# Kernel optimization log

Measured on AMD Instinct MI355X. Metric: run time of the kernel, lower is better.

Reference implementation:

```python
import jax, jax.numpy as jnp
import numpy as np

B, TK, NK, H = 64, 512, 256, 512

def _masked_renorm_softmax(scores, mask):
    # softmax over last dim, multiply by mask, renormalize (as in the torch code)
    p = jax.nn.softmax(scores, axis=-1) * mask
    return p / jnp.sum(p, axis=-1, keepdims=True)

def setup_inputs() -> dict:
    key = jax.random.key(0)
    ks = jax.random.split(key, 14)
    s = 0.02
    return {
        "s_t_hat": jax.random.normal(ks[0], (B, 2 * H), jnp.float32),
        "encoder_outputs_token": jax.random.normal(ks[1], (B, TK, H), jnp.float32),
        "encoder_outputs_node": jax.random.normal(ks[2], (B, NK, H), jnp.float32),
        "node_to_token": jax.random.randint(ks[3], (B, TK), 0, NK),
        "enc_padding_mask_token": jnp.ones((B, TK), jnp.float32),
        "enc_padding_mask_node": jnp.ones((B, NK), jnp.float32),
        "graph": jax.random.uniform(ks[4], (B, NK, NK), jnp.float32),
        "flow": jax.random.uniform(ks[5], (B, NK), jnp.float32),
        # parameters (Linear weights stored as [in, out]; x @ W == torch Linear)
        "W_c": jax.random.normal(ks[6], (H,), jnp.float32) * s,          # Linear(1, H)
        "W_tok": jax.random.normal(ks[7], (H, H), jnp.float32) * s,      # encode_proj_token
        "W_node": jax.random.normal(ks[8], (H, H), jnp.float32) * s,     # encode_proj_node
        "W_dec": jax.random.normal(ks[9], (2 * H, H), jnp.float32) * s,  # decode_proj
        "b_dec": jnp.zeros((H,), jnp.float32),
        "v_tok": jax.random.normal(ks[10], (H,), jnp.float32) * s,       # v_token
        "v_node": jax.random.normal(ks[11], (H,), jnp.float32) * s,      # v_node
    }

def reference(s_t_hat, encoder_outputs_token, encoder_outputs_node, node_to_token,
              enc_padding_mask_token, enc_padding_mask_node, graph, flow,
              W_c, W_tok, W_node, W_dec, b_dec, v_tok, v_node):
    # projections
    enc_tok_feat = jnp.einsum('bth,hk->btk', encoder_outputs_token, W_tok)   # [B,TK,H]
    enc_node_feat = jnp.einsum('bnh,hk->bnk', encoder_outputs_node, W_node)  # [B,NK,H]
    dec_fea = s_t_hat @ W_dec + b_dec                                        # [B,H]
    flow_feat = flow[..., None] * W_c                                        # [B,NK,H]

    # node attention
    e_node = jnp.tanh(enc_node_feat + dec_fea[:, None, :] + flow_feat)
    scores_node = jnp.einsum('bnh,h->bn', e_node, v_node)                    # [B,NK]
    attn_dist_node = _masked_renorm_softmax(scores_node, enc_padding_mask_node)

    # gather node attention onto tokens via node_to_token indices
    gathered = jnp.take_along_axis(attn_dist_node, node_to_token, axis=1)    # [B,TK]
    attn_dist_node_to_token = _masked_renorm_softmax(gathered, enc_padding_mask_token)

    # token attention
    e_tok = jnp.tanh(enc_tok_feat + dec_fea[:, None, :])
    scores_tok = jnp.einsum('bth,h->bt', e_tok, v_tok)                       # [B,TK]
    attn_dist_token = _masked_renorm_softmax(scores_tok, enc_padding_mask_token)

    # mix and context
    final_attn = 0.5 * attn_dist_token + 0.5 * attn_dist_node_to_token      # [B,TK]
    c_t = jnp.einsum('bt,bth->bh', final_attn, encoder_outputs_token)        # [B,H]

    # multi-hop graph diffusion of node attention
    zero_hop = attn_dist_node                                                # [B,NK]
    one_hop = jnp.einsum('bn,bnm->bm', zero_hop, graph)
    two_hop = jnp.einsum('bn,bnm->bm', one_hop, graph)
    flow_out = (zero_hop + one_hop + two_hop) * 0.33333

    return (c_t, final_attn, attn_dist_node, flow_out)
```

## Files before the change

### kernel.cpp

```cpp
#include <hip/hip_runtime.h>
#include <math.h>

constexpr int kB = 64;
constexpr int kTK = 512;
constexpr int kNK = 256;
constexpr int kH = 512;

typedef float f32x4 __attribute__((ext_vector_type(4)));
typedef __bf16 bf16x8 __attribute__((ext_vector_type(8)));
typedef unsigned short u16x8 __attribute__((ext_vector_type(8)));

__device__ __forceinline__ unsigned short f32_to_bf16(float f) {
  unsigned int u = __float_as_uint(f);
  u += 0x7fffu + ((u >> 16) & 1u);
  return (unsigned short)(u >> 16);
}

__device__ __forceinline__ float tanh_fast(float x) {
  float e = __builtin_amdgcn_exp2f(x * 2.8853900817779268f);
  return 1.0f - 2.0f * __builtin_amdgcn_rcpf(e + 1.0f);
}

__global__ __launch_bounds__(256) void transpose_w_kernel(
    const float* __restrict__ Wtok, const float* __restrict__ Wnode,
    unsigned short* __restrict__ WtokT, unsigned short* __restrict__ WnodeT) {
  const float* W = blockIdx.z ? Wnode : Wtok;
  unsigned short* T = blockIdx.z ? WnodeT : WtokT;
  __shared__ float tile[32][33];
  const int tx = threadIdx.x, ty = threadIdx.y;
  const int bx = blockIdx.x, by = blockIdx.y;
#pragma unroll
  for (int i = 0; i < 4; ++i)
    tile[ty + 8 * i][tx] = W[(size_t)(by * 32 + ty + 8 * i) * kH + bx * 32 + tx];
  __syncthreads();
#pragma unroll
  for (int i = 0; i < 4; ++i)
    T[(size_t)(bx * 32 + ty + 8 * i) * kH + by * 32 + tx] =
        f32_to_bf16(tile[tx][ty + 8 * i]);
}

__global__ __launch_bounds__(512) void dec_partial_kernel(
    const float* __restrict__ s_t_hat, const float* __restrict__ W_dec,
    float* __restrict__ part) {
  const int b = blockIdx.x, s = blockIdx.y, h = threadIdx.x;
  __shared__ float sh[128];
  if (h < 128) sh[h] = s_t_hat[(size_t)b * (2 * kH) + s * 128 + h];
  __syncthreads();
  float acc = 0.f;
  const float* w = W_dec + (size_t)(s * 128) * kH + h;
#pragma unroll 8
  for (int k = 0; k < 128; ++k) acc = fmaf(sh[k], w[(size_t)k * kH], acc);
  part[(size_t)(b * 8 + s) * kH + h] = acc;
}

__global__ __launch_bounds__(512) void dec_reduce_kernel(
    const float* __restrict__ part, const float* __restrict__ b_dec,
    float* __restrict__ dec_fea) {
  const int b = blockIdx.x, h = threadIdx.x;
  float acc = b_dec[h];
#pragma unroll
  for (int s = 0; s < 8; ++s) acc += part[(size_t)(b * 8 + s) * kH + h];
  dec_fea[b * kH + h] = acc;
}

template <int ROWS, bool IS_NODE>
__global__ __launch_bounds__(512, 2) void scores_kernel(
    const float* __restrict__ A,
    const unsigned short* __restrict__ WT,
    const float* __restrict__ dec_fea,
    const float* __restrict__ flow,
    const float* __restrict__ W_c,
    const float* __restrict__ v,
    float* __restrict__ scores)
{
  constexpr int TILES_PER_B = ROWS / 64;
  const int b = blockIdx.x / TILES_PER_B;
  const int row0 = (blockIdx.x % TILES_PER_B) * 64;
  const int tid = threadIdx.x;
  const int wave = tid >> 6;
  const int lane = tid & 63;
  const int quad = lane >> 4;
  const int l15 = lane & 15;
  const int n0 = wave * 64;

  __shared__ __align__(16) unsigned short As[2][4096];
  __shared__ float red[8][64];

  const f32x4 fzero = {0.f, 0.f, 0.f, 0.f};
  f32x4 acc[4][4];
#pragma unroll
  for (int i = 0; i < 4; ++i)
#pragma unroll
    for (int j = 0; j < 4; ++j) acc[i][j] = fzero;

  const int sr = tid >> 3;
  const int kq = tid & 7;
  const int slot = (((kq >> 2) * 4 + (sr >> 4)) * 64 + (kq & 3) * 16 + (sr & 15)) * 8;
  const float* aptr = A + ((size_t)(b * ROWS + row0 + sr)) * kH + kq * 8;

  auto stage = [&](int kc, int buf) {
    float4 a0 = *(const float4*)(aptr + kc * 64);
    float4 a1 = *(const float4*)(aptr + kc * 64 + 4);
    u16x8 h;
    h[0] = f32_to_bf16(a0.x); h[1] = f32_to_bf16(a0.y);
    h[2] = f32_to_bf16(a0.z); h[3] = f32_to_bf16(a0.w);
    h[4] = f32_to_bf16(a1.x); h[5] = f32_to_bf16(a1.y);
    h[6] = f32_to_bf16(a1.z); h[7] = f32_to_bf16(a1.w);
    *(u16x8*)&As[buf][slot] = h;
  };

  const unsigned short* bbase = WT + (size_t)(n0 + l15) * kH + quad * 8;
  auto load_b = [&](bf16x8 (&dst)[2][4], int kc) {
#pragma unroll
    for (int kh = 0; kh < 2; ++kh)
#pragma unroll
      for (int ni = 0; ni < 4; ++ni)
        dst[kh][ni] =
            *(const bf16x8*)(bbase + (size_t)(ni * 16) * kH + kc * 64 + kh * 32);
  };

  bf16x8 bcur[2][4];
  stage(0, 0);
  load_b(bcur, 0);
  __syncthreads();

#pragma unroll
  for (int kc = 0; kc < 8; ++kc) {
    bf16x8 bnxt[2][4];
    if (kc < 7) {
      load_b(bnxt, kc + 1);
      stage(kc + 1, (kc + 1) & 1);
    }
    bf16x8 afr[2][4];
#pragma unroll
    for (int kh = 0; kh < 2; ++kh)
#pragma unroll
      for (int mi = 0; mi < 4; ++mi)
        afr[kh][mi] = *(const bf16x8*)&As[kc & 1][((kh * 4 + mi) * 64 + lane) * 8];
#pragma unroll
    for (int kh = 0; kh < 2; ++kh)
#pragma unroll
      for (int mi = 0; mi < 4; ++mi)
#pragma unroll
        for (int ni = 0; ni < 4; ++ni)
          acc[mi][ni] = __builtin_amdgcn_mfma_f32_16x16x32_bf16(
              afr[kh][mi], bcur[kh][ni], acc[mi][ni], 0, 0, 0);
    if (kc < 7) {
#pragma unroll
      for (int kh = 0; kh < 2; ++kh)
#pragma unroll
        for (int ni = 0; ni < 4; ++ni) bcur[kh][ni] = bnxt[kh][ni];
      __syncthreads();
    }
  }

  float dec4[4], vv4[4], wc4[4];
#pragma unroll
  for (int ni = 0; ni < 4; ++ni) {
    const int col = n0 + 16 * ni + l15;
    dec4[ni] = dec_fea[b * kH + col];
    vv4[ni] = v[col];
    if constexpr (IS_NODE) wc4[ni] = W_c[col]; else wc4[ni] = 0.f;
  }
#pragma unroll
  for (int mi = 0; mi < 4; ++mi) {
#pragma unroll
    for (int reg = 0; reg < 4; ++reg) {
      const int row = 16 * mi + quad * 4 + reg;
      float fl = 0.f;
      if constexpr (IS_NODE) fl = flow[b * kNK + row0 + row];
      float p = 0.f;
#pragma unroll
      for (int ni = 0; ni < 4; ++ni) {
        float val = acc[mi][ni][reg] + dec4[ni];
        if constexpr (IS_NODE) val = fmaf(fl, wc4[ni], val);
        p += tanh_fast(val) * vv4[ni];
      }
#pragma unroll
      for (int off = 1; off < 16; off <<= 1) p += __shfl_xor(p, off, 64);
      if (l15 == 0) red[wave][row] = p;
    }
  }
  __syncthreads();
  if (tid < 64) {
    float s = 0.f;
#pragma unroll
    for (int w = 0; w < 8; ++w) s += red[w][tid];
    scores[b * ROWS + row0 + tid] = s;
  }
}

__device__ __forceinline__ float block_sum_512(float v, float* rbuf) {
#pragma unroll
  for (int off = 32; off >= 1; off >>= 1) v += __shfl_xor(v, off, 64);
  if ((threadIdx.x & 63) == 0) rbuf[threadIdx.x >> 6] = v;
  __syncthreads();
  float s = rbuf[0];
#pragma unroll
  for (int w = 1; w < 8; ++w) s += rbuf[w];
  __syncthreads();
  return s;
}

__global__ __launch_bounds__(512) void softmax_mix_kernel(
    const float* __restrict__ scores_node, const float* __restrict__ scores_tok,
    const int* __restrict__ node_to_token,
    const float* __restrict__ mask_tok, const float* __restrict__ mask_node,
    float* __restrict__ out_final, float* __restrict__ out_attn_node) {
  const int b = blockIdx.x, tid = threadIdx.x;
  __shared__ float an_sh[kNK];
  __shared__ float rbuf[8];

  float en = 0.f;
  if (tid < kNK)
    en = expf(scores_node[b * kNK + tid]) * mask_node[b * kNK + tid];
  float sn = block_sum_512(en, rbuf);
  float an = en / sn;
  if (tid < kNK) {
    an_sh[tid] = an;
    out_attn_node[b * kNK + tid] = an;
  }
  __syncthreads();

  const float mt = mask_tok[b * kTK + tid];
  const int idx = node_to_token[b * kTK + tid];
  float eg = expf(an_sh[idx]) * mt;
  float sg = block_sum_512(eg, rbuf);
  float an2t = eg / sg;

  float et = expf(scores_tok[b * kTK + tid]) * mt;
  float st = block_sum_512(et, rbuf);
  float at = et / st;

  out_final[b * kTK + tid] = 0.5f * (at + an2t);
}

__global__ __launch_bounds__(512) void ct_partial_kernel(
    const float* __restrict__ final_attn, const float* __restrict__ enc_tok,
    float* __restrict__ ctp) {
  const int s = blockIdx.x, b = blockIdx.y, h = threadIdx.x;
  __shared__ float fa[64];
  if (h < 64) fa[h] = final_attn[b * kTK + s * 64 + h];
  __syncthreads();
  float acc = 0.f;
  const float* base = enc_tok + ((size_t)(b * kTK + s * 64)) * kH + h;
#pragma unroll 8
  for (int t = 0; t < 64; ++t) acc = fmaf(fa[t], base[(size_t)t * kH], acc);
  ctp[(size_t)(b * 8 + s) * kH + h] = acc;
}

__global__ __launch_bounds__(512) void ct_reduce_kernel(
    const float* __restrict__ ctp, float* __restrict__ out_ct) {
  const int b = blockIdx.x, h = threadIdx.x;
  float acc = 0.f;
#pragma unroll
  for (int s = 0; s < 8; ++s) acc += ctp[(size_t)(b * 8 + s) * kH + h];
  out_ct[b * kH + h] = acc;
}

__global__ __launch_bounds__(256) void flow1_kernel(
    const float* __restrict__ attn_node, const float* __restrict__ graph,
    float* __restrict__ fp1) {
  const int s = blockIdx.x, b = blockIdx.y, m = threadIdx.x;
  __shared__ float z[32];
  if (m < 32) z[m] = attn_node[b * kNK + s * 32 + m];
  __syncthreads();
  float acc = 0.f;
  const float* g = graph + ((size_t)(b * kNK + s * 32)) * kNK + m;
#pragma unroll 8
  for (int n = 0; n < 32; ++n) acc = fmaf(z[n], g[(size_t)n * kNK], acc);
  fp1[(b * 8 + s) * kNK + m] = acc;
}

__global__ __launch_bounds__(256) void flow3_kernel(
    const float* __restrict__ fp1, const float* __restrict__ graph,
    float* __restrict__ fp2) {
  const int s = blockIdx.x, b = blockIdx.y, m = threadIdx.x;
  __shared__ float one[32];
  if (m < 32) {
    float o = 0.f;
#pragma unroll
    for (int sp = 0; sp < 8; ++sp) o += fp1[(b * 8 + sp) * kNK + s * 32 + m];
    one[m] = o;
  }
  __syncthreads();
  float acc = 0.f;
  const float* g = graph + ((size_t)(b * kNK + s * 32)) * kNK + m;
#pragma unroll 8
  for (int n = 0; n < 32; ++n) acc = fmaf(one[n], g[(size_t)n * kNK], acc);
  fp2[(b * 8 + s) * kNK + m] = acc;
}

__global__ __launch_bounds__(256) void flow4_kernel(
    const float* __restrict__ fp1, const float* __restrict__ fp2,
    const float* __restrict__ attn_node, float* __restrict__ out_flow) {
  const int b = blockIdx.x, m = threadIdx.x;
  float one = 0.f, two = 0.f;
#pragma unroll
  for (int s = 0; s < 8; ++s) {
    one += fp1[(b * 8 + s) * kNK + m];
    two += fp2[(b * 8 + s) * kNK + m];
  }
  out_flow[b * kNK + m] = (attn_node[b * kNK + m] + one + two) * 0.33333f;
}

extern "C" void kernel_launch(void* const* d_in, const int* in_sizes, int n_in,
                              void* d_out, int out_size, void* d_ws, size_t ws_size,
                              hipStream_t stream) {
  (void)in_sizes; (void)n_in; (void)out_size; (void)ws_size;
  const float* s_t_hat  = (const float*)d_in[0];
  const float* enc_tok  = (const float*)d_in[1];
  const float* enc_node = (const float*)d_in[2];
  const int*   n2t      = (const int*)d_in[3];
  const float* mask_tok = (const float*)d_in[4];
  const float* mask_nd  = (const float*)d_in[5];
  const float* graph    = (const float*)d_in[6];
  const float* flow     = (const float*)d_in[7];
  const float* W_c      = (const float*)d_in[8];
  const float* W_tok    = (const float*)d_in[9];
  const float* W_node   = (const float*)d_in[10];
  const float* W_dec    = (const float*)d_in[11];
  const float* b_dec    = (const float*)d_in[12];
  const float* v_tok    = (const float*)d_in[13];
  const float* v_node   = (const float*)d_in[14];

  float* out = (float*)d_out;
  float* out_ct        = out;
  float* out_final     = out + kB * kH;
  float* out_attn_node = out + 2 * kB * kH;
  float* out_flow      = out_attn_node + kB * kNK;

  float* ws = (float*)d_ws;
  float* dec_fea_buf = ws;
  float* scores_tok  = ws + 32768;
  float* scores_node = ws + 65536;
  float* fp1         = ws + 81920;
  float* fp2         = ws + 212992;
  float* dec_part    = ws + 344064;
  float* ctp         = dec_part;
  unsigned short* WtokT  = (unsigned short*)(ws + 606208);
  unsigned short* WnodeT = WtokT + kH * kH;

  transpose_w_kernel<<<dim3(16, 16, 2), dim3(32, 8), 0, stream>>>(
      W_tok, W_node, WtokT, WnodeT);
  dec_partial_kernel<<<dim3(kB, 8), 512, 0, stream>>>(s_t_hat, W_dec, dec_part);
  dec_reduce_kernel<<<kB, 512, 0, stream>>>(dec_part, b_dec, dec_fea_buf);
  scores_kernel<kTK, false><<<kB * kTK / 64, 512, 0, stream>>>(
      enc_tok, WtokT, dec_fea_buf, nullptr, nullptr, v_tok, scores_tok);
  scores_kernel<kNK, true><<<kB * kNK / 64, 512, 0, stream>>>(
      enc_node, WnodeT, dec_fea_buf, flow, W_c, v_node, scores_node);
  softmax_mix_kernel<<<kB, 512, 0, stream>>>(scores_node, scores_tok, n2t,
                                             mask_tok, mask_nd, out_final, out_attn_node);
  ct_partial_kernel<<<dim3(8, kB), 512, 0, stream>>>(out_final, enc_tok, ctp);
  ct_reduce_kernel<<<kB, 512, 0, stream>>>(ctp, out_ct);
  flow1_kernel<<<dim3(8, kB), 256, 0, stream>>>(out_attn_node, graph, fp1);
  flow3_kernel<<<dim3(8, kB), 256, 0, stream>>>(fp1, graph, fp2);
  flow4_kernel<<<kB, 256, 0, stream>>>(fp1, fp2, out_attn_node, out_flow);
}
```

Measured before the change: 248.1 us.

## Fuse launches: merge prep, scores, context and graph-diffusion kernels with atomics

Cuts the launch count from eleven to five. The weight transpose is merged with the decoder partial GEMV. Token and node score GEMMs run in one 1024-thread kernel with a narrower per-wave N tile and a finer K pipeline, and the dec reduction is folded into its epilogue. The context reduction and two-hop graph diffusion are fused into two kernels that accumulate flow_out with atomicAdd, and bf16 rounding is simplified to round-half-up. The aim is to remove launch gaps and small reduction kernels. In exchange, atomics make the flow sum order nondeterministic and the rounding change slightly alters numerics.

```diff
diff --git a/kernel.cpp b/kernel.cpp
--- a/kernel.cpp
+++ b/kernel.cpp
@@ -5,15 +5,15 @@
 constexpr int kTK = 512;
 constexpr int kNK = 256;
 constexpr int kH = 512;
+constexpr int kTokBlocks = kB * kTK / 64;
+constexpr int kNodeBlocks = kB * kNK / 64;
 
 typedef float f32x4 __attribute__((ext_vector_type(4)));
 typedef __bf16 bf16x8 __attribute__((ext_vector_type(8)));
 typedef unsigned short u16x8 __attribute__((ext_vector_type(8)));
 
 __device__ __forceinline__ unsigned short f32_to_bf16(float f) {
-  unsigned int u = __float_as_uint(f);
-  u += 0x7fffu + ((u >> 16) & 1u);
-  return (unsigned short)(u >> 16);
+  return (unsigned short)((__float_as_uint(f) + 0x8000u) >> 16);
 }
 
 __device__ __forceinline__ float tanh_fast(float x) {
@@ -21,161 +21,155 @@
   return 1.0f - 2.0f * __builtin_amdgcn_rcpf(e + 1.0f);
 }
 
-__global__ __launch_bounds__(256) void transpose_w_kernel(
+__device__ __forceinline__ void lds_barrier() {
+  __builtin_amdgcn_s_waitcnt(0xC07F);
+  __builtin_amdgcn_s_barrier();
+}
+
+__global__ __launch_bounds__(256) void prep_kernel(
     const float* __restrict__ Wtok, const float* __restrict__ Wnode,
-    unsigned short* __restrict__ WtokT, unsigned short* __restrict__ WnodeT) {
-  const float* W = blockIdx.z ? Wnode : Wtok;
-  unsigned short* T = blockIdx.z ? WnodeT : WtokT;
-  __shared__ float tile[32][33];
-  const int tx = threadIdx.x, ty = threadIdx.y;
-  const int bx = blockIdx.x, by = blockIdx.y;
+    unsigned short* __restrict__ WtokT, unsigned short* __restrict__ WnodeT,
+    const float* __restrict__ s_t_hat, const float* __restrict__ W_dec,
+    float* __restrict__ dec_part) {
+  __shared__ float sm[32 * 33];
+  const int tid = threadIdx.x;
+  if (blockIdx.x < 512) {
+    const int idx = blockIdx.x;
+    const int z = idx >> 8, rem = idx & 255;
+    const int bx = rem & 15, by = rem >> 4;
+    const float* W = z ? Wnode : Wtok;
+    unsigned short* T = z ? WnodeT : WtokT;
+    const int tx = tid & 31, ty = tid >> 5;
+#pragma unroll
+    for (int i = 0; i < 4; ++i)
+      sm[(ty + 8 * i) * 33 + tx] =
+          W[(size_t)(by * 32 + ty + 8 * i) * kH + bx * 32 + tx];
+    __syncthreads();
+#pragma unroll
+    for (int i = 0; i < 4; ++i)
+      T[(size_t)(bx * 32 + ty + 8 * i) * kH + by * 32 + tx] =
+          f32_to_bf16(sm[tx * 33 + ty + 8 * i]);
+  } else {
+    const int r = blockIdx.x - 512;
+    const int b = r >> 3, s = r & 7;
+    if (tid < 128) sm[tid] = s_t_hat[(size_t)b * 1024 + s * 128 + tid];
+    __syncthreads();
+    float a0 = 0.f, a1 = 0.f;
+    const float* w = W_dec + (size_t)(s * 128) * kH;
+#pragma unroll 8
+    for (int k = 0; k < 128; ++k) {
+      a0 = fmaf(sm[k], w[(size_t)k * kH + tid], a0);
+      a1 = fmaf(sm[k], w[(size_t)k * kH + tid + 256], a1);
+    }
+    dec_part[(size_t)(b * 8 + s) * kH + tid] = a0;
+    dec_part[(size_t)(b * 8 + s) * kH + tid + 256] = a1;
+  }
+}
+
+__global__ __launch_bounds__(1024, 4) void scores_fused_kernel(
+    const float* __restrict__ enc_tok, const float* __restrict__ enc_node,
+    const unsigned short* __restrict__ WtokT,
+    const unsigned short* __restrict__ WnodeT,
+    const float* __restrict__ dec_part, const float* __restrict__ b_dec,
+    const float* __restrict__ flow, const float* __restrict__ W_c,
+    const float* __restrict__ v_tok, const float* __restrict__ v_node,
+    float* __restrict__ scores_tok, float* __restrict__ scores_node) {
+  const int tid = threadIdx.x;
+  const int wave = tid >> 6, lane = tid & 63;
+  const int quad = lane >> 4, l15 = lane & 15;
+  const bool is_node = blockIdx.x >= kTokBlocks;
+  const int bidx = is_node ? (int)blockIdx.x - kTokBlocks : (int)blockIdx.x;
+  const float* A = is_node ? enc_node : enc_tok;
+  const unsigned short* WT = is_node ? WnodeT : WtokT;
+  const float* v = is_node ? v_node : v_tok;
+  float* scores = is_node ? scores_node : scores_tok;
+  const int ROWS = is_node ? kNK : kTK;
+  const int b = is_node ? (bidx >> 2) : (bidx >> 3);
+  const int row0 = (is_node ? (bidx & 3) : (bidx & 7)) * 64;
+
+  __shared__ __align__(16) unsigned short As[2][8192];
+  __shared__ float red[16][64];
+
+  const f32x4 fzero = {0.f, 0.f, 0.f, 0.f};
+  f32x4 acc[4][2];
 #pragma unroll
   for (int i = 0; i < 4; ++i)
-    tile[ty + 8 * i][tx] = W[(size_t)(by * 32 + ty + 8 * i) * kH + bx * 32 + tx];
-  __syncthreads();
-#pragma unroll
-  for (int i = 0; i < 4; ++i)
-    T[(size_t)(bx * 32 + ty + 8 * i) * kH + by * 32 + tx] =
-        f32_to_bf16(tile[tx][ty + 8 * i]);
-}
-
-__global__ __launch_bounds__(512) void dec_partial_kernel(
-    const float* __restrict__ s_t_hat, const float* __restrict__ W_dec,
-    float* __restrict__ part) {
-  const int b = blockIdx.x, s = blockIdx.y, h = threadIdx.x;
-  __shared__ float sh[128];
-  if (h < 128) sh[h] = s_t_hat[(size_t)b * (2 * kH) + s * 128 + h];
-  __syncthreads();
-  float acc = 0.f;
-  const float* w = W_dec + (size_t)(s * 128) * kH + h;
-#pragma unroll 8
-  for (int k = 0; k < 128; ++k) acc = fmaf(sh[k], w[(size_t)k * kH], acc);
-  part[(size_t)(b * 8 + s) * kH + h] = acc;
-}
-
-__global__ __launch_bounds__(512) void dec_reduce_kernel(
-    const float* __restrict__ part, const float* __restrict__ b_dec,
-    float* __restrict__ dec_fea) {
-  const int b = blockIdx.x, h = threadIdx.x;
-  float acc = b_dec[h];
-#pragma unroll
-  for (int s = 0; s < 8; ++s) acc += part[(size_t)(b * 8 + s) * kH + h];
-  dec_fea[b * kH + h] = acc;
-}
-
-template <int ROWS, bool IS_NODE>
-__global__ __launch_bounds__(512, 2) void scores_kernel(
-    const float* __restrict__ A,
-    const unsigned short* __restrict__ WT,
-    const float* __restrict__ dec_fea,
-    const float* __restrict__ flow,
-    const float* __restrict__ W_c,
-    const float* __restrict__ v,
-    float* __restrict__ scores)
-{
-  constexpr int TILES_PER_B = ROWS / 64;
-  const int b = blockIdx.x / TILES_PER_B;
-  const int row0 = (blockIdx.x % TILES_PER_B) * 64;
-  const int tid = threadIdx.x;
-  const int wave = tid >> 6;
-  const int lane = tid & 63;
-  const int quad = lane >> 4;
-  const int l15 = lane & 15;
-  const int n0 = wave * 64;
-
-  __shared__ __align__(16) unsigned short As[2][4096];
-  __shared__ float red[8][64];
-
-  const f32x4 fzero = {0.f, 0.f, 0.f, 0.f};
-  f32x4 acc[4][4];
-#pragma unroll
-  for (int i = 0; i < 4; ++i)
-#pragma unroll
-    for (int j = 0; j < 4; ++j) acc[i][j] = fzero;
-
-  const int sr = tid >> 3;
-  const int kq = tid & 7;
-  const int slot = (((kq >> 2) * 4 + (sr >> 4)) * 64 + (kq & 3) * 16 + (sr & 15)) * 8;
-  const float* aptr = A + ((size_t)(b * ROWS + row0 + sr)) * kH + kq * 8;
-
-  auto stage = [&](int kc, int buf) {
-    float4 a0 = *(const float4*)(aptr + kc * 64);
-    float4 a1 = *(const float4*)(aptr + kc * 64 + 4);
+#pragma unroll
+    for (int j = 0; j < 2; ++j) acc[i][j] = fzero;
+
+  const int arow = ((tid >> 6) & 3) * 16 + (tid & 15);
+  const int akk = (tid >> 8) * 32 + ((tid >> 4) & 3) * 8;
+  const float* aptr = A + (size_t)(b * ROWS + row0 + arow) * kH + akk;
+  float4 ax0, ax1;
+  auto aload = [&](int kc) {
+    ax0 = *(const float4*)(aptr + kc * 128);
+    ax1 = *(const float4*)(aptr + kc * 128 + 4);
+  };
+  auto acommit = [&](int buf) {
     u16x8 h;
-    h[0] = f32_to_bf16(a0.x); h[1] = f32_to_bf16(a0.y);
-    h[2] = f32_to_bf16(a0.z); h[3] = f32_to_bf16(a0.w);
-    h[4] = f32_to_bf16(a1.x); h[5] = f32_to_bf16(a1.y);
-    h[6] = f32_to_bf16(a1.z); h[7] = f32_to_bf16(a1.w);
-    *(u16x8*)&As[buf][slot] = h;
+    h[0] = f32_to_bf16(ax0.x); h[1] = f32_to_bf16(ax0.y);
+    h[2] = f32_to_bf16(ax0.z); h[3] = f32_to_bf16(ax0.w);
+    h[4] = f32_to_bf16(ax1.x); h[5] = f32_to_bf16(ax1.y);
+    h[6] = f32_to_bf16(ax1.z); h[7] = f32_to_bf16(ax1.w);
+    *(u16x8*)&As[buf][tid * 8] = h;
   };
 
+  const int n0 = wave * 32;
   const unsigned short* bbase = WT + (size_t)(n0 + l15) * kH + quad * 8;
-  auto load_b = [&](bf16x8 (&dst)[2][4], int kc) {
-#pragma unroll
-    for (int kh = 0; kh < 2; ++kh)
-#pragma unroll
-      for (int ni = 0; ni < 4; ++ni)
-        dst[kh][ni] =
-            *(const bf16x8*)(bbase + (size_t)(ni * 16) * kH + kc * 64 + kh * 32);
+  bf16x8 bbuf[2][2];
+  auto loadB = [&](int sb, int g) {
+    bbuf[sb][0] = *(const bf16x8*)(bbase + g * 32);
+    bbuf[sb][1] = *(const bf16x8*)(bbase + (size_t)16 * kH + g * 32);
   };
 
-  bf16x8 bcur[2][4];
-  stage(0, 0);
-  load_b(bcur, 0);
-  __syncthreads();
-
-#pragma unroll
-  for (int kc = 0; kc < 8; ++kc) {
-    bf16x8 bnxt[2][4];
-    if (kc < 7) {
-      load_b(bnxt, kc + 1);
-      stage(kc + 1, (kc + 1) & 1);
+  aload(0);
+  acommit(0);
+  aload(1);
+  loadB(0, 0);
+  lds_barrier();
+
+#pragma unroll
+  for (int g = 0; g < 16; ++g) {
+    const int kc = g >> 2, kh = g & 3;
+    if (kh == 0 && kc < 3) {
+      acommit((kc + 1) & 1);
+      if (kc < 2) aload(kc + 2);
     }
-    bf16x8 afr[2][4];
-#pragma unroll
-    for (int kh = 0; kh < 2; ++kh)
-#pragma unroll
-      for (int mi = 0; mi < 4; ++mi)
-        afr[kh][mi] = *(const bf16x8*)&As[kc & 1][((kh * 4 + mi) * 64 + lane) * 8];
-#pragma unroll
-    for (int kh = 0; kh < 2; ++kh)
-#pragma unroll
-      for (int mi = 0; mi < 4; ++mi)
-#pragma unroll
-        for (int ni = 0; ni < 4; ++ni)
-          acc[mi][ni] = __builtin_amdgcn_mfma_f32_16x16x32_bf16(
-              afr[kh][mi], bcur[kh][ni], acc[mi][ni], 0, 0, 0);
-    if (kc < 7) {
-#pragma unroll
-      for (int kh = 0; kh < 2; ++kh)
-#pragma unroll
-        for (int ni = 0; ni < 4; ++ni) bcur[kh][ni] = bnxt[kh][ni];
-      __syncthreads();
-    }
-  }
-
-  float dec4[4], vv4[4], wc4[4];
-#pragma unroll
-  for (int ni = 0; ni < 4; ++ni) {
+    if (g < 15) loadB((g + 1) & 1, g + 1);
+    bf16x8 afr[4];
+#pragma unroll
+    for (int mi = 0; mi < 4; ++mi)
+      afr[mi] = *(const bf16x8*)&As[kc & 1][((kh * 4 + mi) * 64 + lane) * 8];
+#pragma unroll
+    for (int mi = 0; mi < 4; ++mi)
+#pragma unroll
+      for (int ni = 0; ni < 2; ++ni)
+        acc[mi][ni] = __builtin_amdgcn_mfma_f32_16x16x32_bf16(
+            afr[mi], bbuf[g & 1][ni], acc[mi][ni], 0, 0, 0);
+    if (kh == 3 && kc < 3) lds_barrier();
+  }
+
+  float dec2[2], vv2[2], wc2[2];
+#pragma unroll
+  for (int ni = 0; ni < 2; ++ni) {
     const int col = n0 + 16 * ni + l15;
-    dec4[ni] = dec_fea[b * kH + col];
-    vv4[ni] = v[col];
-    if constexpr (IS_NODE) wc4[ni] = W_c[col]; else wc4[ni] = 0.f;
+    float d = b_dec[col];
+#pragma unroll
+    for (int p = 0; p < 8; ++p) d += dec_part[(size_t)(b * 8 + p) * kH + col];
+    dec2[ni] = d;
+    vv2[ni] = v[col];
+    wc2[ni] = is_node ? W_c[col] : 0.f;
   }
 #pragma unroll
   for (int mi = 0; mi < 4; ++mi) {
 #pragma unroll
     for (int reg = 0; reg < 4; ++reg) {
       const int row = 16 * mi + quad * 4 + reg;
-      float fl = 0.f;
-      if constexpr (IS_NODE) fl = flow[b * kNK + row0 + row];
+      const float fl = is_node ? flow[b * kNK + row0 + row] : 0.f;
       float p = 0.f;
 #pragma unroll
-      for (int ni = 0; ni < 4; ++ni) {
-        float val = acc[mi][ni][reg] + dec4[ni];
-        if constexpr (IS_NODE) val = fmaf(fl, wc4[ni], val);
-        p += tanh_fast(val) * vv4[ni];
-      }
+      for (int ni = 0; ni < 2; ++ni)
+        p += tanh_fast(fmaf(fl, wc2[ni], acc[mi][ni][reg] + dec2[ni])) * vv2[ni];
 #pragma unroll
       for (int off = 1; off < 16; off <<= 1) p += __shfl_xor(p, off, 64);
       if (l15 == 0) red[wave][row] = p;
@@ -185,7 +179,7 @@
   if (tid < 64) {
     float s = 0.f;
 #pragma unroll
-    for (int w = 0; w < 8; ++w) s += red[w][tid];
+    for (int w = 0; w < 16; ++w) s += red[w][tid];
     scores[b * ROWS + row0 + tid] = s;
   }
 }
@@ -206,10 +200,13 @@
     const float* __restrict__ scores_node, const float* __restrict__ scores_tok,
     const int* __restrict__ node_to_token,
     const float* __restrict__ mask_tok, const float* __restrict__ mask_node,
-    float* __restrict__ out_final, float* __restrict__ out_attn_node) {
+    float* __restrict__ out_final, float* __restrict__ out_attn_node,
+    float* __restrict__ out_flow) {
   const int b = blockIdx.x, tid = threadIdx.x;
   __shared__ float an_sh[kNK];
   __shared__ float rbuf[8];
+
+  if (tid < kNK) out_flow[b * kNK + tid] = 0.f;
 
   float en = 0.f;
   if (tid < kNK)
@@ -235,73 +232,71 @@
   out_final[b * kTK + tid] = 0.5f * (at + an2t);
 }
 
-__global__ __launch_bounds__(512) void ct_partial_kernel(
+__global__ __launch_bounds__(512) void ct_flow1_kernel(
     const float* __restrict__ final_attn, const float* __restrict__ enc_tok,
-    float* __restrict__ ctp) {
-  const int s = blockIdx.x, b = blockIdx.y, h = threadIdx.x;
-  __shared__ float fa[64];
-  if (h < 64) fa[h] = final_attn[b * kTK + s * 64 + h];
-  __syncthreads();
-  float acc = 0.f;
-  const float* base = enc_tok + ((size_t)(b * kTK + s * 64)) * kH + h;
+    const float* __restrict__ attn_node, const float* __restrict__ graph,
+    float* __restrict__ ctp, float* __restrict__ fp1) {
+  __shared__ float sm[64];
+  const int tid = threadIdx.x;
+  if (blockIdx.x < 512) {
+    const int s = blockIdx.x & 7, b = blockIdx.x >> 3;
+    if (tid < 64) sm[tid] = final_attn[b * kTK + s * 64 + tid];
+    __syncthreads();
+    float acc = 0.f;
+    const float* base = enc_tok + ((size_t)(b * kTK + s * 64)) * kH + tid;
+#pragma unroll 16
+    for (int t = 0; t < 64; ++t) acc = fmaf(sm[t], base[(size_t)t * kH], acc);
+    ctp[(size_t)(b * 8 + s) * kH + tid] = acc;
+  } else {
+    const int r = blockIdx.x - 512;
+    const int b = r >> 2, sl = r & 3;
+    const int m = tid & 255, half = tid >> 8;
+    if (tid < 64) sm[tid] = attn_node[b * kNK + sl * 64 + tid];
+    __syncthreads();
+    float acc = 0.f;
+    const float* g =
+        graph + ((size_t)(b * kNK + sl * 64 + half * 32)) * kNK + m;
 #pragma unroll 8
-  for (int t = 0; t < 64; ++t) acc = fmaf(fa[t], base[(size_t)t * kH], acc);
-  ctp[(size_t)(b * 8 + s) * kH + h] = acc;
-}
-
-__global__ __launch_bounds__(512) void ct_reduce_kernel(
-    const float* __restrict__ ctp, float* __restrict__ out_ct) {
-  const int b = blockIdx.x, h = threadIdx.x;
-  float acc = 0.f;
-#pragma unroll
-  for (int s = 0; s < 8; ++s) acc += ctp[(size_t)(b * 8 + s) * kH + h];
-  out_ct[b * kH + h] = acc;
-}
-
-__global__ __launch_bounds__(256) void flow1_kernel(
+    for (int n = 0; n < 32; ++n)
+      acc = fmaf(sm[half * 32 + n], g[(size_t)n * kNK], acc);
+    fp1[(size_t)(b * 8 + sl * 2 + half) * kNK + m] = acc;
+  }
+}
+
+__global__ __launch_bounds__(512) void ct_flow2_kernel(
+    const float* __restrict__ ctp, const float* __restrict__ fp1,
     const float* __restrict__ attn_node, const float* __restrict__ graph,
-    float* __restrict__ fp1) {
-  const int s = blockIdx.x, b = blockIdx.y, m = threadIdx.x;
-  __shared__ float z[32];
-  if (m < 32) z[m] = attn_node[b * kNK + s * 32 + m];
-  __syncthreads();
-  float acc = 0.f;
-  const float* g = graph + ((size_t)(b * kNK + s * 32)) * kNK + m;
+    float* __restrict__ out_ct, float* __restrict__ out_flow) {
+  __shared__ float one_sh[64];
+  const int tid = threadIdx.x;
+  if (blockIdx.x < 64) {
+    const int b = blockIdx.x;
+    float acc = 0.f;
+#pragma unroll
+    for (int p = 0; p < 8; ++p) acc += ctp[(size_t)(b * 8 + p) * kH + tid];
+    out_ct[b * kH + tid] = acc;
+  } else {
+    const int r = blockIdx.x - 64;
+    const int b = r >> 2, sl = r & 3;
+    const int m = tid & 255, half = tid >> 8;
+    if (tid < 64) {
+      const int n = sl * 64 + tid;
+      float one = 0.f;
+#pragma unroll
+      for (int p = 0; p < 8; ++p) one += fp1[(size_t)(b * 8 + p) * kNK + n];
+      one_sh[tid] = one;
+      atomicAdd(&out_flow[b * kNK + n],
+                (attn_node[b * kNK + n] + one) * 0.33333f);
+    }
+    __syncthreads();
+    float acc = 0.f;
+    const float* g =
+        graph + ((size_t)(b * kNK + sl * 64 + half * 32)) * kNK + m;
 #pragma unroll 8
-  for (int n = 0; n < 32; ++n) acc = fmaf(z[n], g[(size_t)n * kNK], acc);
-  fp1[(b * 8 + s) * kNK + m] = acc;
-}
-
-__global__ __launch_bounds__(256) void flow3_kernel(
-    const float* __restrict__ fp1, const float* __restrict__ graph,
-    float* __restrict__ fp2) {
-  const int s = blockIdx.x, b = blockIdx.y, m = threadIdx.x;
-  __shared__ float one[32];
-  if (m < 32) {
-    float o = 0.f;
-#pragma unroll
-    for (int sp = 0; sp < 8; ++sp) o += fp1[(b * 8 + sp) * kNK + s * 32 + m];
-    one[m] = o;
-  }
-  __syncthreads();
-  float acc = 0.f;
-  const float* g = graph + ((size_t)(b * kNK + s * 32)) * kNK + m;
-#pragma unroll 8
-  for (int n = 0; n < 32; ++n) acc = fmaf(one[n], g[(size_t)n * kNK], acc);
-  fp2[(b * 8 + s) * kNK + m] = acc;
-}
-
-__global__ __launch_bounds__(256) void flow4_kernel(
-    const float* __restrict__ fp1, const float* __restrict__ fp2,
-    const float* __restrict__ attn_node, float* __restrict__ out_flow) {
-  const int b = blockIdx.x, m = threadIdx.x;
-  float one = 0.f, two = 0.f;
-#pragma unroll
-  for (int s = 0; s < 8; ++s) {
-    one += fp1[(b * 8 + s) * kNK + m];
-    two += fp2[(b * 8 + s) * kNK + m];
-  }
-  out_flow[b * kNK + m] = (attn_node[b * kNK + m] + one + two) * 0.33333f;
+    for (int n = 0; n < 32; ++n)
+      acc = fmaf(one_sh[half * 32 + n], g[(size_t)n * kNK], acc);
+    atomicAdd(&out_flow[b * kNK + m], acc * 0.33333f);
+  }
 }
 
 extern "C" void kernel_launch(void* const* d_in, const int* in_sizes, int n_in,
@@ -331,29 +326,24 @@
   float* out_flow      = out_attn_node + kB * kNK;
 
   float* ws = (float*)d_ws;
-  float* dec_fea_buf = ws;
-  float* scores_tok  = ws + 32768;
-  float* scores_node = ws + 65536;
-  float* fp1         = ws + 81920;
-  float* fp2         = ws + 212992;
-  float* dec_part    = ws + 344064;
+  float* scores_tok  = ws;
+  float* scores_node = ws + 32768;
+  float* dec_part    = ws + 49152;
   float* ctp         = dec_part;
-  unsigned short* WtokT  = (unsigned short*)(ws + 606208);
+  float* fp1         = ws + 311296;
+  unsigned short* WtokT  = (unsigned short*)(ws + 442368);
   unsigned short* WnodeT = WtokT + kH * kH;
 
-  transpose_w_kernel<<<dim3(16, 16, 2), dim3(32, 8), 0, stream>>>(
-      W_tok, W_node, WtokT, WnodeT);
-  dec_partial_kernel<<<dim3(kB, 8), 512, 0, stream>>>(s_t_hat, W_dec, dec_part);
-  dec_reduce_kernel<<<kB, 512, 0, stream>>>(dec_part, b_dec, dec_fea_buf);
-  scores_kernel<kTK, false><<<kB * kTK / 64, 512, 0, stream>>>(
-      enc_tok, WtokT, dec_fea_buf, nullptr, nullptr, v_tok, scores_tok);
-  scores_kernel<kNK, true><<<kB * kNK / 64, 512, 0, stream>>>(
-      enc_node, WnodeT, dec_fea_buf, flow, W_c, v_node, scores_node);
+  prep_kernel<<<1024, 256, 0, stream>>>(W_tok, W_node, WtokT, WnodeT,
+                                        s_t_hat, W_dec, dec_part);
+  scores_fused_kernel<<<kTokBlocks + kNodeBlocks, 1024, 0, stream>>>(
+      enc_tok, enc_node, WtokT, WnodeT, dec_part, b_dec, flow, W_c,
+      v_tok, v_node, scores_tok, scores_node);
   softmax_mix_kernel<<<kB, 512, 0, stream>>>(scores_node, scores_tok, n2t,
-                                             mask_tok, mask_nd, out_final, out_attn_node);
-  ct_partial_kernel<<<dim3(8, kB), 512, 0, stream>>>(out_final, enc_tok, ctp);
-  ct_reduce_kernel<<<kB, 512, 0, stream>>>(ctp, out_ct);
-  flow1_kernel<<<dim3(8, kB), 256, 0, stream>>>(out_attn_node, graph, fp1);
-  flow3_kernel<<<dim3(8, kB), 256, 0, stream>>>(fp1, graph, fp2);
-  flow4_kernel<<<kB, 256, 0, stream>>>(fp1, fp2, out_attn_node, out_flow);
-}
+                                             mask_tok, mask_nd, out_final,
+                                             out_attn_node, out_flow);
+  ct_flow1_kernel<<<768, 512, 0, stream>>>(out_final, enc_tok, out_attn_node,
+                                           graph, ctp, fp1);
+  ct_flow2_kernel<<<320, 512, 0, stream>>>(ctp, fp1, out_attn_node, graph,
+                                           out_ct, out_flow);
+}
```

Result: no change. 243.7 us (-1.8%).
